# Performance work log

Measured on AMD Instinct MI355X. Metric: run time of the kernel, lower is better.

The kernel has to match this reference:

```python
import jax, jax.numpy as jnp
import numpy as np


def setup_inputs() -> dict:
    key = jax.random.key(0)
    k1, k2 = jax.random.split(key)
    n, t, c, l = 32, 64, 256, 64
    query = jax.random.normal(k1, (n, t, c, l), dtype=jnp.float32)
    key_t = jax.random.normal(k2, (t, n, c), dtype=jnp.float32)
    return {"query": query, "key": key_t}


def reference(query, key):
    # scores[n,l] = sum_{t,c} query[n,t,c,l] * key[t,n,c]
    scores = jnp.einsum('ntcl,tnc->nl', query, key)
    scores = jax.nn.softmax(scores, axis=1)
    # out[t,n,c] = sum_l query[n,t,c,l] * scores[n,l]
    out = jnp.einsum('ntcl,nl->tnc', query, scores)
    return out
```

## Files before the change

### kernel.cpp

```cpp
#include <hip/hip_runtime.h>

#define N 32
#define T 64
#define C 256
#define L 64
#define TC (T * C)
#define BLK_PER_N 64
#define PAIRS_PER_BLK (TC / BLK_PER_N)

__global__ __launch_bounds__(256, 8) void scores_partial_kernel(
    const float* __restrict__ q, const float* __restrict__ k,
    float* __restrict__ partial) {
  const int n    = blockIdx.y;
  const int tid  = threadIdx.x;
  const int lane = tid & 63;
  const int wave = tid >> 6;
  const int sub  = lane >> 4;
  const int lq   = lane & 15;
  const int g    = wave * 4 + sub;

  const int p0 = blockIdx.x * PAIRS_PER_BLK;
  const float* qn = q + (size_t)n * TC * L;

  float4 acc = make_float4(0.f, 0.f, 0.f, 0.f);
  #pragma unroll 4
  for (int i = g; i < PAIRS_PER_BLK; i += 16) {
    const int p = p0 + i;
    const float4 qv = *reinterpret_cast<const float4*>(qn + (size_t)p * L + lq * 4);
    const int t = p >> 8;
    const int c = p & 255;
    const float kv = k[t * (N * C) + n * C + c];
    acc.x = fmaf(qv.x, kv, acc.x);
    acc.y = fmaf(qv.y, kv, acc.y);
    acc.z = fmaf(qv.z, kv, acc.z);
    acc.w = fmaf(qv.w, kv, acc.w);
  }

  acc.x += __shfl_xor(acc.x, 16); acc.y += __shfl_xor(acc.y, 16);
  acc.z += __shfl_xor(acc.z, 16); acc.w += __shfl_xor(acc.w, 16);
  acc.x += __shfl_xor(acc.x, 32); acc.y += __shfl_xor(acc.y, 32);
  acc.z += __shfl_xor(acc.z, 32); acc.w += __shfl_xor(acc.w, 32);

  __shared__ float sdata[4 * L];
  if (lane < 16) {
    sdata[wave * L + lq * 4 + 0] = acc.x;
    sdata[wave * L + lq * 4 + 1] = acc.y;
    sdata[wave * L + lq * 4 + 2] = acc.z;
    sdata[wave * L + lq * 4 + 3] = acc.w;
  }
  __syncthreads();
  if (tid < L) {
    const float s = sdata[tid] + sdata[L + tid] + sdata[2 * L + tid] + sdata[3 * L + tid];
    partial[(size_t)blockIdx.x * (N * L) + n * L + tid] = s;
  }
}

__global__ __launch_bounds__(256, 8) void out_kernel(
    const float* __restrict__ q, const float* __restrict__ partial,
    float* __restrict__ out) {
  const int n    = blockIdx.y;
  const int tid  = threadIdx.x;
  const int lane = tid & 63;
  const int wave = tid >> 6;

  __shared__ float sred[4 * L];
  __shared__ float probs[L];
  {
    float s = 0.f;
    #pragma unroll 4
    for (int b = wave * 16; b < wave * 16 + 16; ++b)
      s += partial[(size_t)b * (N * L) + n * L + lane];
    sred[wave * L + lane] = s;
  }
  __syncthreads();
  if (tid < L) {
    float s = sred[tid] + sred[L + tid] + sred[2 * L + tid] + sred[3 * L + tid];
    float m = s;
    #pragma unroll
    for (int off = 32; off > 0; off >>= 1) m = fmaxf(m, __shfl_xor(m, off));
    const float e = __expf(s - m);
    float sum = e;
    #pragma unroll
    for (int off = 32; off > 0; off >>= 1) sum += __shfl_xor(sum, off);
    probs[tid] = e / sum;
  }
  __syncthreads();

  const int sub = lane >> 4;
  const int lq  = lane & 15;
  const int g   = wave * 4 + sub;

  const float4 pv = *reinterpret_cast<const float4*>(&probs[lq * 4]);
  const int p0 = blockIdx.x * PAIRS_PER_BLK;
  const float* qn = q + (size_t)n * TC * L;

  #pragma unroll 4
  for (int i = g; i < PAIRS_PER_BLK; i += 16) {
    const int p = p0 + i;
    const float4 qv = *reinterpret_cast<const float4*>(qn + (size_t)p * L + lq * 4);
    float d = qv.x * pv.x + qv.y * pv.y + qv.z * pv.z + qv.w * pv.w;
    d += __shfl_xor(d, 1);
    d += __shfl_xor(d, 2);
    d += __shfl_xor(d, 4);
    d += __shfl_xor(d, 8);
    if (lq == 0) {
      const int t = p >> 8;
      const int c = p & 255;
      out[t * (N * C) + n * C + c] = d;
    }
  }
}

extern "C" void kernel_launch(void* const* d_in, const int* in_sizes, int n_in,
                              void* d_out, int out_size, void* d_ws, size_t ws_size,
                              hipStream_t stream) {
  const float* q = (const float*)d_in[0];
  const float* k = (const float*)d_in[1];
  float* out = (float*)d_out;
  float* partial = (float*)d_ws;

  dim3 grid(BLK_PER_N, N);
  scores_partial_kernel<<<grid, 256, 0, stream>>>(q, k, partial);
  out_kernel<<<grid, 256, 0, stream>>>(q, partial, out);
}
```

Baseline: 211.5 us.

## Fuse scores and output passes into one cooperative kernel with grid sync

Replaces the two-kernel pipeline with one cooperative kernel. Each block computes partial scores for two time steps, with the key vectors staged in shared memory, then a grid-wide barrier is hit. Each block then reduces the 32 partials per batch, applies softmax and writes the output rows. This removes a kernel launch and the separate 64-way partial buffer, but it relies on all 1024 blocks being co-resident and adds a grid-sync cost. The old two-kernel path is kept as a fallback if the cooperative launch fails.

```diff
diff --git a/kernel.cpp b/kernel.cpp
--- a/kernel.cpp
+++ b/kernel.cpp
@@ -1,4 +1,7 @@
 #include <hip/hip_runtime.h>
+#include <hip/hip_cooperative_groups.h>
+
+namespace cg = cooperative_groups;
 
 #define N 32
 #define T 64
@@ -7,6 +10,104 @@
 #define TC (T * C)
 #define BLK_PER_N 64
 #define PAIRS_PER_BLK (TC / BLK_PER_N)
+
+__global__ __launch_bounds__(256, 4) void fused_attn_kernel(
+    const float* __restrict__ q, const float* __restrict__ k,
+    float* __restrict__ partial, float* __restrict__ out) {
+  const int n    = blockIdx.y;
+  const int bx   = blockIdx.x;
+  const int tid  = threadIdx.x;
+  const int lane = tid & 63;
+  const int wave = tid >> 6;
+  const int sub  = lane >> 4;
+  const int lq   = lane & 15;
+  const int g    = wave * 4 + sub;
+
+  __shared__ float sk[2 * C];
+  __shared__ float sred[4 * L];
+  __shared__ __align__(16) float probs[L];
+
+  sk[tid]     = k[(bx * N + n) * C + tid];
+  sk[C + tid] = k[((bx + 32) * N + n) * C + tid];
+  __syncthreads();
+
+  float4 acc = make_float4(0.f, 0.f, 0.f, 0.f);
+  #pragma unroll
+  for (int half = 0; half < 2; ++half) {
+    const int t = bx + half * 32;
+    const float* __restrict__ qrow =
+        q + ((size_t)(n * T + t) * C) * L + lq * 4;
+    const float* __restrict__ skr = sk + half * C;
+    #pragma unroll 4
+    for (int c = g; c < C; c += 16) {
+      const float4 qv = *reinterpret_cast<const float4*>(qrow + (size_t)c * L);
+      const float kv = skr[c];
+      acc.x = fmaf(qv.x, kv, acc.x);
+      acc.y = fmaf(qv.y, kv, acc.y);
+      acc.z = fmaf(qv.z, kv, acc.z);
+      acc.w = fmaf(qv.w, kv, acc.w);
+    }
+  }
+  acc.x += __shfl_xor(acc.x, 16); acc.y += __shfl_xor(acc.y, 16);
+  acc.z += __shfl_xor(acc.z, 16); acc.w += __shfl_xor(acc.w, 16);
+  acc.x += __shfl_xor(acc.x, 32); acc.y += __shfl_xor(acc.y, 32);
+  acc.z += __shfl_xor(acc.z, 32); acc.w += __shfl_xor(acc.w, 32);
+
+  if (lane < 16) {
+    sred[wave * L + lq * 4 + 0] = acc.x;
+    sred[wave * L + lq * 4 + 1] = acc.y;
+    sred[wave * L + lq * 4 + 2] = acc.z;
+    sred[wave * L + lq * 4 + 3] = acc.w;
+  }
+  __syncthreads();
+  if (tid < L) {
+    const float s = sred[tid] + sred[L + tid] + sred[2 * L + tid] + sred[3 * L + tid];
+    partial[((size_t)n * 32 + bx) * L + tid] = s;
+  }
+  __threadfence();
+  cg::this_grid().sync();
+
+  {
+    float s = 0.f;
+    const float* __restrict__ pn = partial + (size_t)n * (32 * L);
+    #pragma unroll
+    for (int b = wave * 8; b < wave * 8 + 8; ++b)
+      s += pn[b * L + lane];
+    sred[wave * L + lane] = s;
+  }
+  __syncthreads();
+  if (tid < L) {
+    float v = sred[tid] + sred[L + tid] + sred[2 * L + tid] + sred[3 * L + tid];
+    float m = v;
+    #pragma unroll
+    for (int off = 32; off > 0; off >>= 1) m = fmaxf(m, __shfl_xor(m, off));
+    const float e = __expf(v - m);
+    float z = e;
+    #pragma unroll
+    for (int off = 32; off > 0; off >>= 1) z += __shfl_xor(z, off);
+    probs[tid] = e / z;
+  }
+  __syncthreads();
+
+  const float4 pv = *reinterpret_cast<const float4*>(&probs[lq * 4]);
+  #pragma unroll
+  for (int half = 0; half < 2; ++half) {
+    const int t = bx + half * 32;
+    const float* __restrict__ qrow =
+        q + ((size_t)(n * T + t) * C) * L + lq * 4;
+    float* __restrict__ orow = out + (size_t)(t * N + n) * C;
+    #pragma unroll 4
+    for (int c = g; c < C; c += 16) {
+      const float4 qv = *reinterpret_cast<const float4*>(qrow + (size_t)c * L);
+      float d = qv.x * pv.x + qv.y * pv.y + qv.z * pv.z + qv.w * pv.w;
+      d += __shfl_xor(d, 1);
+      d += __shfl_xor(d, 2);
+      d += __shfl_xor(d, 4);
+      d += __shfl_xor(d, 8);
+      if (lq == 0) orow[c] = d;
+    }
+  }
+}
 
 __global__ __launch_bounds__(256, 8) void scores_partial_kernel(
     const float* __restrict__ q, const float* __restrict__ k,
@@ -35,7 +136,6 @@
     acc.z = fmaf(qv.z, kv, acc.z);
     acc.w = fmaf(qv.w, kv, acc.w);
   }
-
   acc.x += __shfl_xor(acc.x, 16); acc.y += __shfl_xor(acc.y, 16);
   acc.z += __shfl_xor(acc.z, 16); acc.w += __shfl_xor(acc.w, 16);
   acc.x += __shfl_xor(acc.x, 32); acc.y += __shfl_xor(acc.y, 32);
@@ -64,7 +164,7 @@
   const int wave = tid >> 6;
 
   __shared__ float sred[4 * L];
-  __shared__ float probs[L];
+  __shared__ __align__(16) float probs[L];
   {
     float s = 0.f;
     #pragma unroll 4
@@ -119,7 +219,13 @@
   float* out = (float*)d_out;
   float* partial = (float*)d_ws;
 
-  dim3 grid(BLK_PER_N, N);
-  scores_partial_kernel<<<grid, 256, 0, stream>>>(q, k, partial);
-  out_kernel<<<grid, 256, 0, stream>>>(q, partial, out);
-}
+  dim3 grid(T / 2, N);
+  void* args[] = {(void*)&q, (void*)&k, (void*)&partial, (void*)&out};
+  hipError_t err = hipLaunchCooperativeKernel(
+      (const void*)fused_attn_kernel, grid, dim3(256), args, 0, stream);
+  if (err != hipSuccess) {
+    dim3 g2(BLK_PER_N, N);
+    scores_partial_kernel<<<g2, 256, 0, stream>>>(q, k, partial);
+    out_kernel<<<g2, 256, 0, stream>>>(q, partial, out);
+  }
+}
```

Measured after the change: 394.8 us. +86.7%, slower.

## Map blocks to (t,n) rows, stage key in LDS, per-thread row dot in out kernel

Applied to the files above, without the earlier changes.

Both kernels now assign one block per (t,n) pair instead of a flat pair range. The scores kernel loads that block's 256 key values into LDS with a single coalesced load, replacing scattered global key reads. The out kernel gives each thread one full 64-float query row and does the dot product serially, dropping the shuffle reductions and giving coalesced output writes. The trade-off is that each thread's query reads are strided 256 bytes apart across lanes, which weakens load coalescing in the out kernel.

```diff
diff --git a/kernel.cpp b/kernel.cpp
--- a/kernel.cpp
+++ b/kernel.cpp
@@ -4,13 +4,11 @@
 #define T 64
 #define C 256
 #define L 64
-#define TC (T * C)
-#define BLK_PER_N 64
-#define PAIRS_PER_BLK (TC / BLK_PER_N)
 
 __global__ __launch_bounds__(256, 8) void scores_partial_kernel(
     const float* __restrict__ q, const float* __restrict__ k,
     float* __restrict__ partial) {
+  const int t    = blockIdx.x;
   const int n    = blockIdx.y;
   const int tid  = threadIdx.x;
   const int lane = tid & 63;
@@ -19,17 +17,19 @@
   const int lq   = lane & 15;
   const int g    = wave * 4 + sub;
 
-  const int p0 = blockIdx.x * PAIRS_PER_BLK;
-  const float* qn = q + (size_t)n * TC * L;
+  __shared__ float sk[C];
+  __shared__ float sred[4 * L];
+
+  sk[tid] = k[(t * N + n) * C + tid];
+  __syncthreads();
+
+  const float* __restrict__ qrow = q + ((size_t)(n * T + t) * C) * L + lq * 4;
 
   float4 acc = make_float4(0.f, 0.f, 0.f, 0.f);
   #pragma unroll 4
-  for (int i = g; i < PAIRS_PER_BLK; i += 16) {
-    const int p = p0 + i;
-    const float4 qv = *reinterpret_cast<const float4*>(qn + (size_t)p * L + lq * 4);
-    const int t = p >> 8;
-    const int c = p & 255;
-    const float kv = k[t * (N * C) + n * C + c];
+  for (int c = g; c < C; c += 16) {
+    const float4 qv = *reinterpret_cast<const float4*>(qrow + (size_t)c * L);
+    const float kv = sk[c];
     acc.x = fmaf(qv.x, kv, acc.x);
     acc.y = fmaf(qv.y, kv, acc.y);
     acc.z = fmaf(qv.z, kv, acc.z);
@@ -41,30 +41,31 @@
   acc.x += __shfl_xor(acc.x, 32); acc.y += __shfl_xor(acc.y, 32);
   acc.z += __shfl_xor(acc.z, 32); acc.w += __shfl_xor(acc.w, 32);
 
-  __shared__ float sdata[4 * L];
   if (lane < 16) {
-    sdata[wave * L + lq * 4 + 0] = acc.x;
-    sdata[wave * L + lq * 4 + 1] = acc.y;
-    sdata[wave * L + lq * 4 + 2] = acc.z;
-    sdata[wave * L + lq * 4 + 3] = acc.w;
+    sred[wave * L + lq * 4 + 0] = acc.x;
+    sred[wave * L + lq * 4 + 1] = acc.y;
+    sred[wave * L + lq * 4 + 2] = acc.z;
+    sred[wave * L + lq * 4 + 3] = acc.w;
   }
   __syncthreads();
   if (tid < L) {
-    const float s = sdata[tid] + sdata[L + tid] + sdata[2 * L + tid] + sdata[3 * L + tid];
-    partial[(size_t)blockIdx.x * (N * L) + n * L + tid] = s;
+    const float s = sred[tid] + sred[L + tid] + sred[2 * L + tid] + sred[3 * L + tid];
+    partial[(size_t)t * (N * L) + n * L + tid] = s;
   }
 }
 
 __global__ __launch_bounds__(256, 8) void out_kernel(
     const float* __restrict__ q, const float* __restrict__ partial,
     float* __restrict__ out) {
+  const int t    = blockIdx.x;
   const int n    = blockIdx.y;
   const int tid  = threadIdx.x;
   const int lane = tid & 63;
   const int wave = tid >> 6;
 
   __shared__ float sred[4 * L];
-  __shared__ float probs[L];
+  __shared__ __align__(16) float probs[L];
+
   {
     float s = 0.f;
     #pragma unroll 4
@@ -74,41 +75,27 @@
   }
   __syncthreads();
   if (tid < L) {
-    float s = sred[tid] + sred[L + tid] + sred[2 * L + tid] + sred[3 * L + tid];
-    float m = s;
+    float v = sred[tid] + sred[L + tid] + sred[2 * L + tid] + sred[3 * L + tid];
+    float m = v;
     #pragma unroll
     for (int off = 32; off > 0; off >>= 1) m = fmaxf(m, __shfl_xor(m, off));
-    const float e = __expf(s - m);
-    float sum = e;
+    const float e = __expf(v - m);
+    float z = e;
     #pragma unroll
-    for (int off = 32; off > 0; off >>= 1) sum += __shfl_xor(sum, off);
-    probs[tid] = e / sum;
+    for (int off = 32; off > 0; off >>= 1) z += __shfl_xor(z, off);
+    probs[tid] = e / z;
   }
   __syncthreads();
 
-  const int sub = lane >> 4;
-  const int lq  = lane & 15;
-  const int g   = wave * 4 + sub;
-
-  const float4 pv = *reinterpret_cast<const float4*>(&probs[lq * 4]);
-  const int p0 = blockIdx.x * PAIRS_PER_BLK;
-  const float* qn = q + (size_t)n * TC * L;
-
-  #pragma unroll 4
-  for (int i = g; i < PAIRS_PER_BLK; i += 16) {
-    const int p = p0 + i;
-    const float4 qv = *reinterpret_cast<const float4*>(qn + (size_t)p * L + lq * 4);
-    float d = qv.x * pv.x + qv.y * pv.y + qv.z * pv.z + qv.w * pv.w;
-    d += __shfl_xor(d, 1);
-    d += __shfl_xor(d, 2);
-    d += __shfl_xor(d, 4);
-    d += __shfl_xor(d, 8);
-    if (lq == 0) {
-      const int t = p >> 8;
-      const int c = p & 255;
-      out[t * (N * C) + n * C + c] = d;
-    }
+  const float* __restrict__ qrow = q + ((size_t)((n * T + t) * C + tid)) * L;
+  float d = 0.f;
+  #pragma unroll 8
+  for (int lb = 0; lb < 16; ++lb) {
+    const float4 qv = *reinterpret_cast<const float4*>(qrow + lb * 4);
+    const float4 pv = *reinterpret_cast<const float4*>(&probs[lb * 4]);
+    d += qv.x * pv.x + qv.y * pv.y + qv.z * pv.z + qv.w * pv.w;
   }
+  out[(size_t)(t * N + n) * C + tid] = d;
 }
 
 extern "C" void kernel_launch(void* const* d_in, const int* in_sizes, int n_in,
@@ -119,7 +106,7 @@
   float* out = (float*)d_out;
   float* partial = (float*)d_ws;
 
-  dim3 grid(BLK_PER_N, N);
+  dim3 grid(T, N);
   scores_partial_kernel<<<grid, 256, 0, stream>>>(q, k, partial);
   out_kernel<<<grid, 256, 0, stream>>>(q, partial, out);
 }
```

After: 214.0 us. About the same (+1.2%).
